# Performance work log

Measured on AMD Instinct MI355X. Metric: run time of the kernel, lower is better.

The kernel has to match this reference:

```python
import jax, jax.numpy as jnp
import numpy as np

N = 50000   # total nodes
E = 800000  # total edges (avg degree 16)
D = 128     # input_dim == hidden_dim
G = 256     # graphs in batch
C = 16      # output classes
L = 5       # num_layers
BN_EPS = 1e-5


def setup_inputs() -> dict:
    key = jax.random.key(0)
    ks = jax.random.split(key, 8)
    s = 1.0 / np.sqrt(D)
    return {
        "x": jax.random.normal(ks[0], (N, D), dtype=jnp.float32),
        "eps": jnp.zeros((L - 1,), dtype=jnp.float32),
        "W1": jax.random.normal(ks[1], (L - 1, D, D), dtype=jnp.float32) * s,
        "b1": jnp.zeros((L - 1, D), dtype=jnp.float32),
        "g1": jnp.ones((L - 1, D), dtype=jnp.float32),
        "beta1": jnp.zeros((L - 1, D), dtype=jnp.float32),
        "W2": jax.random.normal(ks[2], (L - 1, D, D), dtype=jnp.float32) * s,
        "b2": jnp.zeros((L - 1, D), dtype=jnp.float32),
        "g2": jnp.ones((L - 1, D), dtype=jnp.float32),
        "beta2": jnp.zeros((L - 1, D), dtype=jnp.float32),
        "Wp": jax.random.normal(ks[3], (L, D, C), dtype=jnp.float32) * s,
        "bp": jnp.zeros((L, C), dtype=jnp.float32),
        "edge_src": jax.random.randint(ks[4], (E,), 0, N),
        "edge_dst": jax.random.randint(ks[5], (E,), 0, N),
        "graph_ids": jnp.sort(jax.random.randint(ks[6], (N,), 0, G)),
    }


def _bn(x, g, b):
    # BatchNorm1d in training mode: biased batch statistics over the node axis
    m = jnp.mean(x, axis=0)
    v = jnp.mean(jnp.square(x - m), axis=0)
    return g * (x - m) * jax.lax.rsqrt(v + BN_EPS) + b


def reference(x, eps, W1, b1, g1, beta1, W2, b2, g2, beta2, Wp, bp,
              edge_src, edge_dst, graph_ids):
    hidden_representations = [x]
    h = x
    for l in range(L - 1):
        # spmm(adj, h): gather neighbor features along edges, scatter-add to dst
        pooled = jax.ops.segment_sum(h[edge_src], edge_dst, num_segments=N)
        pooled = pooled + (1.0 + eps[l]) * h  # learn_eps branch
        # MLP (num_mlp_layers=2): Linear+BN+ReLU, then Linear
        z = jax.nn.relu(_bn(pooled @ W1[l] + b1[l], g1[l], beta1[l]))
        z = z @ W2[l] + b2[l]
        # outer BN + ReLU
        h = jax.nn.relu(_bn(z, g2[l], beta2[l]))
        hidden_representations.append(h)

    out = jnp.zeros((G, C), dtype=x.dtype)
    for l, hl in enumerate(hidden_representations):
        # graph_pool spmm: sum-pool node features per graph
        pooled_h = jax.ops.segment_sum(hl, graph_ids, num_segments=G)
        out = out + pooled_h @ Wp[l] + bp[l]  # dropout p=0 -> identity
    return out
```

## Files before the change

kernel.cpp:

```cpp
#include <hip/hip_runtime.h>

#define N_NODES  50000
#define N_EDGES  800000
#define DIM      128
#define N_GRAPHS 256
#define N_CLASSES 16
#define N_LAYERS 5
#define BN_EPS   1e-5f

#define GEMM_BM 64
#define LDSP 136

typedef short bf16x8 __attribute__((ext_vector_type(8)));
typedef float f32x4  __attribute__((ext_vector_type(4)));

__device__ __forceinline__ float bf2f(unsigned short u) {
    unsigned int x = ((unsigned int)u) << 16;
    return __builtin_bit_cast(float, x);
}
__device__ __forceinline__ unsigned short f2bf(float f) {
    unsigned int x = __builtin_bit_cast(unsigned int, f);
    x += 0x7fffu + ((x >> 16) & 1u);
    return (unsigned short)(x >> 16);
}
__device__ __forceinline__ float lo16(unsigned int v) { return bf2f((unsigned short)(v & 0xffffu)); }
__device__ __forceinline__ float hi16(unsigned int v) { return bf2f((unsigned short)(v >> 16)); }
__device__ __forceinline__ unsigned int pack16(float a, float b) {
    return (unsigned int)f2bf(a) | ((unsigned int)f2bf(b) << 16);
}


__global__ void deg_kernel(const int* __restrict__ dst, int* __restrict__ deg, int e_count) {
    int e = blockIdx.x * blockDim.x + threadIdx.x;
    if (e < e_count) atomicAdd(&deg[dst[e]], 1);
}

__global__ void fill_csr_kernel(const int* __restrict__ src, const int* __restrict__ dst,
                                int* __restrict__ cursor, int* __restrict__ csr, int e_count) {
    int e = blockIdx.x * blockDim.x + threadIdx.x;
    if (e < e_count) {
        int d = dst[e];
        int p = atomicAdd(&cursor[d], 1);
        csr[p] = src[e];
    }
}

__global__ void gbound_kernel(const int* __restrict__ gid, int* __restrict__ gptr, int n, int G) {
    int i = blockIdx.x * blockDim.x + threadIdx.x;
    if (i >= n) return;
    int cur = gid[i];
    int prev = (i == 0) ? -1 : gid[i - 1];
    for (int g = prev + 1; g <= cur; ++g) gptr[g] = i;
    if (i == n - 1) {
        for (int g = cur + 1; g <= G; ++g) gptr[g] = n;
    }
}

__global__ void zrow_kernel(unsigned short* __restrict__ a, unsigned short* __restrict__ b) {
    int t = threadIdx.x;
    uint2 z = make_uint2(0u, 0u);
    if (t < 32) ((uint2*)(a + (size_t)N_NODES * DIM))[t] = z;
    else        ((uint2*)(b + (size_t)N_NODES * DIM))[t - 32] = z;
}


__global__ __launch_bounds__(1024) void scan_part_kernel(const int* __restrict__ in,
                                                         int* __restrict__ part, int n) {
    __shared__ int red[16];
    int tid = threadIdx.x;
    int i = blockIdx.x * 1024 + tid;
    int v = (i < n) ? in[i] : 0;
#pragma unroll
    for (int d = 1; d < 64; d <<= 1) v += __shfl_xor(v, d, 64);
    int lane = tid & 63, w = tid >> 6;
    if (lane == 0) red[w] = v;
    __syncthreads();
    if (tid == 0) {
        int s = 0;
#pragma unroll
        for (int k = 0; k < 16; ++k) s += red[k];
        part[blockIdx.x] = s;
    }
}

__global__ void scan_mid_kernel(int* __restrict__ part, int nb,
                                int* __restrict__ total_out, int total_idx) {
    int lane = threadIdx.x;
    int orig = (lane < nb) ? part[lane] : 0;
    int v = orig;
#pragma unroll
    for (int d = 1; d < 64; d <<= 1) {
        int t = __shfl_up(v, d, 64);
        if (lane >= d) v += t;
    }
    if (lane < nb) part[lane] = v - orig;
    if (lane == 63) total_out[total_idx] = v;
}

__global__ __launch_bounds__(1024) void scan_final_kernel(const int* __restrict__ in,
                                                          const int* __restrict__ part,
                                                          int* __restrict__ rowptr,
                                                          int* __restrict__ cursor, int n) {
    __shared__ int woff[16];
    int tid = threadIdx.x;
    int i = blockIdx.x * 1024 + tid;
    int v = (i < n) ? in[i] : 0;
    int lane = tid & 63, w = tid >> 6;
    int x = v;
#pragma unroll
    for (int d = 1; d < 64; d <<= 1) {
        int t = __shfl_up(x, d, 64);
        if (lane >= d) x += t;
    }
    if (lane == 63) woff[w] = x;
    __syncthreads();
    if (tid == 0) {
        int s = 0;
#pragma unroll
        for (int k = 0; k < 16; ++k) { int t = woff[k]; woff[k] = s; s += t; }
    }
    __syncthreads();
    int excl = part[blockIdx.x] + woff[w] + x - v;
    if (i < n) { rowptr[i] = excl; cursor[i] = excl; }
}


__global__ void f2b_kernel(const float* __restrict__ in, unsigned short* __restrict__ outp,
                           int n4d, int n4t) {
    int i = blockIdx.x * blockDim.x + threadIdx.x;
    if (i >= n4t) return;
    uint2 o = make_uint2(0u, 0u);
    if (i < n4d) {
        float4 v = ((const float4*)in)[i];
        o = make_uint2(pack16(v.x, v.y), pack16(v.z, v.w));
    }
    ((uint2*)outp)[i] = o;
}

__global__ void wconv_kernel(const float* __restrict__ W, unsigned short* __restrict__ Wt, int nmat) {
    int t = blockIdx.x * blockDim.x + threadIdx.x;
    if (t >= nmat * DIM * DIM) return;
    int m = t >> 14;
    int rem = t & 16383;
    int k = rem >> 7;
    int c = rem & 127;
    Wt[((size_t)m << 14) + (size_t)c * DIM + k] = f2bf(W[t]);
}


__device__ __forceinline__ void gemm_core8(
    unsigned short (*As)[LDSP], const unsigned short* __restrict__ Wt,
    unsigned short* __restrict__ Z, float* __restrict__ colsum, float* __restrict__ colsumsq,
    int nrows, int row0, int tid)
{
    int wid = tid >> 6, lane = tid & 63;
    int mq = wid & 3, ch = wid >> 2;
    int m0 = mq * 16;
    int lrow = lane & 15;
    int lk = (lane >> 4) * 8;

    f32x4 acc[4];
#pragma unroll
    for (int n = 0; n < 4; ++n) acc[n] = (f32x4){0.f, 0.f, 0.f, 0.f};

#pragma unroll
    for (int kk = 0; kk < 4; ++kk) {
        int k0 = kk * 32;
        bf16x8 a = *(const bf16x8*)&As[m0 + lrow][k0 + lk];
#pragma unroll
        for (int n = 0; n < 4; ++n) {
            bf16x8 b = *(const bf16x8*)(Wt + (size_t)(ch * 64 + n * 16 + lrow) * DIM + k0 + lk);
            acc[n] = __builtin_amdgcn_mfma_f32_16x16x32_bf16(a, b, acc[n], 0, 0, 0);
        }
    }

    int r0 = row0 + m0 + (lane >> 4) * 4;
    float sarr[4], qarr[4];
#pragma unroll
    for (int n = 0; n < 4; ++n) {
        int col = ch * 64 + n * 16 + lrow;
        float s = 0.f, q = 0.f;
#pragma unroll
        for (int j = 0; j < 4; ++j) {
            float v = acc[n][j];
            int row = r0 + j;
            if (row < nrows) Z[(size_t)row * DIM + col] = f2bf(v);
            s += v; q += v * v;
        }
        s += __shfl_xor(s, 16); q += __shfl_xor(q, 16);
        s += __shfl_xor(s, 32); q += __shfl_xor(q, 32);
        sarr[n] = s; qarr[n] = q;
    }

    __syncthreads();
    float* red = (float*)&As[0][0];
    if (lane < 16) {
#pragma unroll
        for (int n = 0; n < 4; ++n) {
            int col = ch * 64 + n * 16 + lrow;
            red[wid * 256 + col]       = sarr[n];
            red[wid * 256 + 128 + col] = qarr[n];
        }
    }
    __syncthreads();
    if (tid < 128) {
        int col = tid;
        int base = (col >> 6) * 4 * 256;
        float ts = red[base + col] + red[base + 256 + col]
                 + red[base + 512 + col] + red[base + 768 + col];
        float tq = red[base + 128 + col] + red[base + 384 + col]
                 + red[base + 640 + col] + red[base + 896 + col];
        atomicAdd(&colsum[col], ts);
        atomicAdd(&colsumsq[col], tq);
    }
}


__global__ __launch_bounds__(512) void gemmA_kernel(
    const unsigned short* __restrict__ h, const int* __restrict__ rowptr,
    const int* __restrict__ csr, const float* __restrict__ epsArr, int l,
    const unsigned short* __restrict__ Wt, unsigned short* __restrict__ Z,
    float* __restrict__ stats, int nrows)
{
    __shared__ __attribute__((aligned(16))) unsigned short As[GEMM_BM][LDSP];
    int tid = threadIdx.x;
    int row0 = blockIdx.x * GEMM_BM;
    int wid = tid >> 6, lane = tid & 63;
    int sub = lane >> 4, chunk = lane & 15;
    float ep = 1.0f + epsArr[l];

    for (int i = 0; i < 8; ++i) {
        int node = row0 + wid * 8 + i;
        float a8[8];
#pragma unroll
        for (int j = 0; j < 8; ++j) a8[j] = 0.f;
        if (node < nrows) {
            int beg = rowptr[node], end = rowptr[node + 1];
            int e0 = beg + sub;
            int sidx[8];
#pragma unroll
            for (int k = 0; k < 8; ++k) {
                int ee = e0 + k * 4;
                int ec = (ee < N_EDGES) ? ee : (N_EDGES - 1);
                int sv = csr[ec];
                sidx[k] = (ee < end) ? sv : N_NODES;
            }
            bf16x8 v[8];
#pragma unroll
            for (int k = 0; k < 8; ++k)
                v[k] = *(const bf16x8*)(h + (size_t)sidx[k] * DIM + chunk * 8);
#pragma unroll
            for (int k = 0; k < 8; ++k)
#pragma unroll
                for (int j = 0; j < 8; ++j)
                    a8[j] += bf2f((unsigned short)v[k][j]);
            for (int e = beg + 32 + sub; e < end; e += 4) {
                int sv = csr[e];
                bf16x8 vv = *(const bf16x8*)(h + (size_t)sv * DIM + chunk * 8);
#pragma unroll
                for (int j = 0; j < 8; ++j) a8[j] += bf2f((unsigned short)vv[j]);
            }
#pragma unroll
            for (int j = 0; j < 8; ++j) {
                a8[j] += __shfl_xor(a8[j], 16);
                a8[j] += __shfl_xor(a8[j], 32);
            }
            bf16x8 hv = *(const bf16x8*)(h + (size_t)node * DIM + chunk * 8);
#pragma unroll
            for (int j = 0; j < 8; ++j) a8[j] += ep * bf2f((unsigned short)hv[j]);
        }
        if (sub == 0) {
            bf16x8 o;
#pragma unroll
            for (int j = 0; j < 8; ++j) o[j] = (short)f2bf(a8[j]);
            *(bf16x8*)&As[wid * 8 + i][chunk * 8] = o;
        }
    }
    __syncthreads();
    gemm_core8(As, Wt, Z, stats, stats + 128, nrows, row0, tid);
}


__global__ __launch_bounds__(512) void gemmB_kernel(
    const unsigned short* __restrict__ Zin, const float* __restrict__ statsIn,
    const float* __restrict__ g, const float* __restrict__ beta,
    const unsigned short* __restrict__ Wt, unsigned short* __restrict__ Zout,
    float* __restrict__ statsOut, int nrows)
{
    __shared__ __attribute__((aligned(16))) unsigned short As[GEMM_BM][LDSP];
    __shared__ float abn[DIM], shbn[DIM];
    int tid = threadIdx.x;
    int row0 = blockIdx.x * GEMM_BM;

    if (tid < DIM) {
        const float invN = 1.0f / (float)N_NODES;
        float m = statsIn[tid] * invN;
        float var = statsIn[128 + tid] * invN - m * m;
        float s = g[tid] * rsqrtf(var + BN_EPS);
        abn[tid] = s;
        shbn[tid] = beta[tid] - s * m;
    }
    __syncthreads();

#pragma unroll
    for (int it = 0; it < 2; ++it) {
        int c = tid + it * 512;
        int r = c >> 4, kc = c & 15;
        bf16x8 o = {0, 0, 0, 0, 0, 0, 0, 0};
        if (row0 + r < nrows) {
            bf16x8 v = *(const bf16x8*)(Zin + (size_t)(row0 + r) * DIM + kc * 8);
#pragma unroll
            for (int cc = 0; cc < 8; ++cc) {
                int col = kc * 8 + cc;
                float f = bf2f((unsigned short)v[cc]);
                f = fmaxf(fmaf(abn[col], f, shbn[col]), 0.f);
                o[cc] = (short)f2bf(f);
            }
        }
        *(bf16x8*)&As[r][kc * 8] = o;
    }
    __syncthreads();
    gemm_core8(As, Wt, Zout, statsOut, statsOut + 128, nrows, row0, tid);
}


__global__ __launch_bounds__(256) void bnpool_kernel(
    const unsigned short* __restrict__ Zin, const float* __restrict__ stats,
    const float* __restrict__ g, const float* __restrict__ beta,
    const int* __restrict__ gid, unsigned short* __restrict__ hout,
    float* __restrict__ pooled, int nrows)
{
    __shared__ float abn[DIM], shbn[DIM];
    int tid = threadIdx.x;
    if (tid < DIM) {
        const float invN = 1.0f / (float)N_NODES;
        float m = stats[tid] * invN;
        float var = stats[128 + tid] * invN - m * m;
        float s = g[tid] * rsqrtf(var + BN_EPS);
        abn[tid] = s;
        shbn[tid] = beta[tid] - s * m;
    }
    __syncthreads();

    int row0 = blockIdx.x * GEMM_BM;
    int lane = tid & 63, w = tid >> 6;
    int c0 = lane * 2;
    float a0 = abn[c0], a1 = abn[c0 + 1], s0 = shbn[c0], s1 = shbn[c0 + 1];
    const unsigned int* Z2 = (const unsigned int*)Zin;
    unsigned int* H2 = (unsigned int*)hout;

    float px = 0.f, py = 0.f;
    int gcur = -1;
    for (int i = 0; i < 16; ++i) {
        int r = row0 + w * 16 + i;
        if (r >= nrows) break;
        int gg = gid[r];
        if (gg != gcur) {
            if (gcur >= 0) {
                atomicAdd(&pooled[(size_t)gcur * DIM + c0], px);
                atomicAdd(&pooled[(size_t)gcur * DIM + c0 + 1], py);
            }
            gcur = gg; px = 0.f; py = 0.f;
        }
        unsigned int v = Z2[(size_t)r * 64 + lane];
        float f0 = fmaxf(fmaf(a0, lo16(v), s0), 0.f);
        float f1 = fmaxf(fmaf(a1, hi16(v), s1), 0.f);
        unsigned int o = pack16(f0, f1);
        H2[(size_t)r * 64 + lane] = o;
        px += lo16(o);
        py += hi16(o);
    }
    if (gcur >= 0) {
        atomicAdd(&pooled[(size_t)gcur * DIM + c0], px);
        atomicAdd(&pooled[(size_t)gcur * DIM + c0 + 1], py);
    }
}


__global__ __launch_bounds__(256) void pool_kernel(
    const float* __restrict__ h, const int* __restrict__ gptr, float* __restrict__ outp)
{
    __shared__ float red[DIM];
    int g = blockIdx.x;
    int c = threadIdx.x & 127;
    int half = threadIdx.x >> 7;
    int beg = gptr[g], end = gptr[g + 1];
    float acc = 0.f;
    for (int n = beg + half; n < end; n += 2) acc += h[(size_t)n * DIM + c];
    if (half == 1) red[c] = acc;
    __syncthreads();
    if (half == 0) outp[(size_t)g * DIM + c] = acc + red[c];
}


__global__ __launch_bounds__(256) void final_kernel(
    const float* __restrict__ pooledH, const float* __restrict__ Wp,
    const float* __restrict__ bp, float* __restrict__ outp)
{
    int t = blockIdx.x * blockDim.x + threadIdx.x;
    if (t >= N_GRAPHS * N_CLASSES) return;
    int g = t >> 4, c = t & 15;
    float acc = 0.f;
    for (int l = 0; l < N_LAYERS; ++l) {
        const float* ph = pooledH + ((size_t)l * N_GRAPHS + g) * DIM;
        const float* w = Wp + (size_t)l * DIM * N_CLASSES + c;
        float a = 0.f;
        for (int k = 0; k < DIM; ++k) a = fmaf(ph[k], w[k * N_CLASSES], a);
        acc += a + bp[l * N_CLASSES + c];
    }
    outp[t] = acc;
}


extern "C" void kernel_launch(void* const* d_in, const int* in_sizes, int n_in,
                              void* d_out, int out_size, void* d_ws, size_t ws_size,
                              hipStream_t stream) {
    const float* x     = (const float*)d_in[0];
    const float* eps   = (const float*)d_in[1];
    const float* W1    = (const float*)d_in[2];
    const float* g1    = (const float*)d_in[4];
    const float* beta1 = (const float*)d_in[5];
    const float* W2    = (const float*)d_in[6];
    const float* g2    = (const float*)d_in[8];
    const float* beta2 = (const float*)d_in[9];
    const float* Wp    = (const float*)d_in[10];
    const float* bp    = (const float*)d_in[11];
    const int*   esrc  = (const int*)d_in[12];
    const int*   edst  = (const int*)d_in[13];
    const int*   gid   = (const int*)d_in[14];
    float* outp = (float*)d_out;

    char* ws = (char*)d_ws;
    size_t off = 0;
    auto alloc = [&](size_t bytes) {
        char* p = ws + off;
        off = (off + bytes + 255) & ~(size_t)255;
        return p;
    };
    unsigned short* xb  = (unsigned short*)alloc((size_t)(N_NODES + 1) * DIM * 2);
    unsigned short* B0  = (unsigned short*)alloc((size_t)(N_NODES + 1) * DIM * 2);
    unsigned short* B1  = (unsigned short*)alloc((size_t)(N_NODES + 1) * DIM * 2);
    unsigned short* ZB  = (unsigned short*)alloc((size_t)N_NODES * DIM * 2);
    unsigned short* Z2B = (unsigned short*)alloc((size_t)N_NODES * DIM * 2);
    unsigned short* Wt1 = (unsigned short*)alloc((size_t)(N_LAYERS - 1) * DIM * DIM * 2);
    unsigned short* Wt2 = (unsigned short*)alloc((size_t)(N_LAYERS - 1) * DIM * DIM * 2);
    int*   csr     = (int*)alloc((size_t)N_EDGES * 4);
    int*   deg     = (int*)alloc((N_NODES + 1) * 4);
    int*   rowptr  = (int*)alloc((N_NODES + 1) * 4);
    int*   cursor  = (int*)alloc((N_NODES + 1) * 4);
    int*   part    = (int*)alloc(64 * 4);
    int*   growptr = (int*)alloc(300 * 4);
    float* stats   = (float*)alloc(8 * 256 * 4);
    float* pooledH = (float*)alloc((size_t)N_LAYERS * N_GRAPHS * DIM * 4);

    hipMemsetAsync(deg, 0, N_NODES * 4, stream);
    hipMemsetAsync(stats, 0, 8 * 256 * 4, stream);
    hipMemsetAsync(pooledH, 0, (size_t)N_LAYERS * N_GRAPHS * DIM * 4, stream);

    const int nsb = (N_NODES + 1023) / 1024;
    deg_kernel<<<(N_EDGES + 255) / 256, 256, 0, stream>>>(edst, deg, N_EDGES);
    scan_part_kernel<<<nsb, 1024, 0, stream>>>(deg, part, N_NODES);
    scan_mid_kernel<<<1, 64, 0, stream>>>(part, nsb, rowptr, N_NODES);
    scan_final_kernel<<<nsb, 1024, 0, stream>>>(deg, part, rowptr, cursor, N_NODES);
    fill_csr_kernel<<<(N_EDGES + 255) / 256, 256, 0, stream>>>(esrc, edst, cursor, csr, N_EDGES);
    gbound_kernel<<<(N_NODES + 255) / 256, 256, 0, stream>>>(gid, growptr, N_NODES, N_GRAPHS);
    zrow_kernel<<<1, 64, 0, stream>>>(B0, B1);

    const int n4d = N_NODES * DIM / 4;
    const int n4t = (N_NODES + 1) * DIM / 4;
    f2b_kernel<<<(n4t + 255) / 256, 256, 0, stream>>>(x, xb, n4d, n4t);
    wconv_kernel<<<((N_LAYERS - 1) * DIM * DIM + 255) / 256, 256, 0, stream>>>(W1, Wt1, N_LAYERS - 1);
    wconv_kernel<<<((N_LAYERS - 1) * DIM * DIM + 255) / 256, 256, 0, stream>>>(W2, Wt2, N_LAYERS - 1);

    pool_kernel<<<N_GRAPHS, 256, 0, stream>>>(x, growptr, pooledH);

    const int ngrid = (N_NODES + GEMM_BM - 1) / GEMM_BM;
    unsigned short* hb = xb;
    unsigned short* nb = B0;
    for (int l = 0; l < N_LAYERS - 1; ++l) {
        gemmA_kernel<<<ngrid, 512, 0, stream>>>(
            hb, rowptr, csr, eps, l, Wt1 + (size_t)l * DIM * DIM, ZB,
            stats + (size_t)(2 * l) * 256, N_NODES);
        gemmB_kernel<<<ngrid, 512, 0, stream>>>(
            ZB, stats + (size_t)(2 * l) * 256, g1 + l * DIM, beta1 + l * DIM,
            Wt2 + (size_t)l * DIM * DIM, Z2B, stats + (size_t)(2 * l + 1) * 256, N_NODES);
        bnpool_kernel<<<ngrid, 256, 0, stream>>>(
            Z2B, stats + (size_t)(2 * l + 1) * 256, g2 + l * DIM, beta2 + l * DIM,
            gid, nb, pooledH + (size_t)(l + 1) * N_GRAPHS * DIM, N_NODES);

        hb = nb;
        nb = (hb == B0) ? B1 : B0;
    }

    final_kernel<<<(N_GRAPHS * N_CLASSES + 255) / 256, 256, 0, stream>>>(pooledH, Wp, bp, outp);
}
```

Measured before the change: 680.4 us.

## Merge setup kernels and gather two nodes per wavefront in aggregation

Folds the degree count and graph-boundary computation into one kernel, and merges the x/W bf16 conversions and layer-0 pooling into a single multi-role launch, cutting the number of kernel launches. In the aggregation GEMM, each wavefront now gathers two nodes at once, with two lanes per feature chunk instead of four, and unrolls over the first 16 edges. This is meant to give more memory-level parallelism across nodes for the average degree of 16 and to drop one shuffle stage. The tradeoff is a longer serial tail loop for high-degree nodes and less edge-level parallelism per node.

Result: slower. 700.9 us (+3.0%).

```diff
diff --git a/kernel.cpp b/kernel.cpp
--- a/kernel.cpp
+++ b/kernel.cpp
@@ -30,9 +30,17 @@
 }
 
 
-__global__ void deg_kernel(const int* __restrict__ dst, int* __restrict__ deg, int e_count) {
-    int e = blockIdx.x * blockDim.x + threadIdx.x;
-    if (e < e_count) atomicAdd(&deg[dst[e]], 1);
+__global__ void degbound_kernel(const int* __restrict__ dst, int* __restrict__ deg,
+                                const int* __restrict__ gid, int* __restrict__ gptr) {
+    int i = blockIdx.x * blockDim.x + threadIdx.x;
+    if (i < N_EDGES) atomicAdd(&deg[dst[i]], 1);
+    if (i < N_NODES) {
+        int cur = gid[i];
+        int prev = (i == 0) ? -1 : gid[i - 1];
+        for (int g = prev + 1; g <= cur; ++g) gptr[g] = i;
+        if (i == N_NODES - 1)
+            for (int g = cur + 1; g <= N_GRAPHS; ++g) gptr[g] = N_NODES;
+    }
 }
 
 __global__ void fill_csr_kernel(const int* __restrict__ src, const int* __restrict__ dst,
@@ -42,17 +50,6 @@
         int d = dst[e];
         int p = atomicAdd(&cursor[d], 1);
         csr[p] = src[e];
-    }
-}
-
-__global__ void gbound_kernel(const int* __restrict__ gid, int* __restrict__ gptr, int n, int G) {
-    int i = blockIdx.x * blockDim.x + threadIdx.x;
-    if (i >= n) return;
-    int cur = gid[i];
-    int prev = (i == 0) ? -1 : gid[i - 1];
-    for (int g = prev + 1; g <= cur; ++g) gptr[g] = i;
-    if (i == n - 1) {
-        for (int g = cur + 1; g <= G; ++g) gptr[g] = n;
     }
 }
 
@@ -125,26 +122,50 @@
 }
 
 
-__global__ void f2b_kernel(const float* __restrict__ in, unsigned short* __restrict__ outp,
-                           int n4d, int n4t) {
-    int i = blockIdx.x * blockDim.x + threadIdx.x;
-    if (i >= n4t) return;
-    uint2 o = make_uint2(0u, 0u);
-    if (i < n4d) {
-        float4 v = ((const float4*)in)[i];
-        o = make_uint2(pack16(v.x, v.y), pack16(v.z, v.w));
-    }
-    ((uint2*)outp)[i] = o;
-}
-
-__global__ void wconv_kernel(const float* __restrict__ W, unsigned short* __restrict__ Wt, int nmat) {
-    int t = blockIdx.x * blockDim.x + threadIdx.x;
-    if (t >= nmat * DIM * DIM) return;
-    int m = t >> 14;
-    int rem = t & 16383;
-    int k = rem >> 7;
-    int c = rem & 127;
-    Wt[((size_t)m << 14) + (size_t)c * DIM + k] = f2bf(W[t]);
+#define CVT_F2B_BLOCKS 2048
+#define CVT_W_BLOCKS   64
+
+__global__ __launch_bounds__(256) void convert_kernel(
+    const float* __restrict__ x, unsigned short* __restrict__ xb,
+    const float* __restrict__ W1, const float* __restrict__ W2,
+    unsigned short* __restrict__ Wt1, unsigned short* __restrict__ Wt2,
+    const int* __restrict__ gptr, float* __restrict__ pool0)
+{
+    __shared__ float red[DIM];
+    int b = blockIdx.x, tid = threadIdx.x;
+    if (b < N_GRAPHS) {
+        int c = tid & 127;
+        int half = tid >> 7;
+        int beg = gptr[b], end = gptr[b + 1];
+        float acc = 0.f;
+        for (int n = beg + half; n < end; n += 2) acc += x[(size_t)n * DIM + c];
+        if (half == 1) red[c] = acc;
+        __syncthreads();
+        if (half == 0) pool0[(size_t)b * DIM + c] = acc + red[c];
+    } else if (b < N_GRAPHS + CVT_F2B_BLOCKS) {
+        const int total_data = N_NODES * DIM / 4;
+        const int total = (N_NODES + 1) * DIM / 4;
+        const int stride = CVT_F2B_BLOCKS * 256;
+        for (int i = (b - N_GRAPHS) * 256 + tid; i < total; i += stride) {
+            uint2 o = make_uint2(0u, 0u);
+            if (i < total_data) {
+                float4 v = ((const float4*)x)[i];
+                o = make_uint2(pack16(v.x, v.y), pack16(v.z, v.w));
+            }
+            ((uint2*)xb)[i] = o;
+        }
+    } else {
+        const int total = (N_LAYERS - 1) * DIM * DIM;
+        const int stride = CVT_W_BLOCKS * 256;
+        for (int t = (b - N_GRAPHS - CVT_F2B_BLOCKS) * 256 + tid; t < total; t += stride) {
+            int m = t >> 14;
+            int k = (t & 16383) >> 7;
+            int c = t & 127;
+            size_t dstp = ((size_t)m << 14) + (size_t)c * DIM + k;
+            Wt1[dstp] = f2bf(W1[t]);
+            Wt2[dstp] = f2bf(W2[t]);
+        }
+    }
 }
 
 
@@ -226,54 +247,60 @@
     int tid = threadIdx.x;
     int row0 = blockIdx.x * GEMM_BM;
     int wid = tid >> 6, lane = tid & 63;
-    int sub = lane >> 4, chunk = lane & 15;
+    int nsel = lane >> 5, esub = (lane >> 4) & 1, chunk = lane & 15;
     float ep = 1.0f + epsArr[l];
 
-    for (int i = 0; i < 8; ++i) {
-        int node = row0 + wid * 8 + i;
+    for (int t = 0; t < 4; ++t) {
+        int node = row0 + wid * 8 + t * 2 + nsel;
+        bool valid = node < nrows;
+        int beg = 0, end = 0;
+        if (valid) { beg = rowptr[node]; end = rowptr[node + 1]; }
+
+        int sidx[8];
+#pragma unroll
+        for (int k = 0; k < 8; ++k) {
+            int ee = beg + esub + 2 * k;
+            int ec = (ee < N_EDGES) ? ee : (N_EDGES - 1);
+            int sv = csr[ec];
+            sidx[k] = (valid && ee < end) ? sv : N_NODES;
+        }
+        bf16x8 v[8];
+#pragma unroll
+        for (int k = 0; k < 8; ++k)
+            v[k] = *(const bf16x8*)(h + (size_t)sidx[k] * DIM + chunk * 8);
+
         float a8[8];
 #pragma unroll
         for (int j = 0; j < 8; ++j) a8[j] = 0.f;
-        if (node < nrows) {
-            int beg = rowptr[node], end = rowptr[node + 1];
-            int e0 = beg + sub;
-            int sidx[8];
-#pragma unroll
-            for (int k = 0; k < 8; ++k) {
-                int ee = e0 + k * 4;
-                int ec = (ee < N_EDGES) ? ee : (N_EDGES - 1);
-                int sv = csr[ec];
-                sidx[k] = (ee < end) ? sv : N_NODES;
-            }
-            bf16x8 v[8];
-#pragma unroll
-            for (int k = 0; k < 8; ++k)
-                v[k] = *(const bf16x8*)(h + (size_t)sidx[k] * DIM + chunk * 8);
-#pragma unroll
-            for (int k = 0; k < 8; ++k)
-#pragma unroll
-                for (int j = 0; j < 8; ++j)
-                    a8[j] += bf2f((unsigned short)v[k][j]);
-            for (int e = beg + 32 + sub; e < end; e += 4) {
+#pragma unroll
+        for (int k = 0; k < 8; ++k)
+#pragma unroll
+            for (int j = 0; j < 8; ++j)
+                a8[j] += bf2f((unsigned short)v[k][j]);
+
+        if (valid) {
+            for (int e = beg + 16 + esub; e < end; e += 2) {
                 int sv = csr[e];
                 bf16x8 vv = *(const bf16x8*)(h + (size_t)sv * DIM + chunk * 8);
 #pragma unroll
                 for (int j = 0; j < 8; ++j) a8[j] += bf2f((unsigned short)vv[j]);
             }
-#pragma unroll
-            for (int j = 0; j < 8; ++j) {
-                a8[j] += __shfl_xor(a8[j], 16);
-                a8[j] += __shfl_xor(a8[j], 32);
-            }
+        }
+
+#pragma unroll
+        for (int j = 0; j < 8; ++j) a8[j] += __shfl_xor(a8[j], 16);
+
+        if (valid) {
             bf16x8 hv = *(const bf16x8*)(h + (size_t)node * DIM + chunk * 8);
 #pragma unroll
             for (int j = 0; j < 8; ++j) a8[j] += ep * bf2f((unsigned short)hv[j]);
         }
-        if (sub == 0) {
+
+        if (esub == 0) {
             bf16x8 o;
 #pragma unroll
             for (int j = 0; j < 8; ++j) o[j] = (short)f2bf(a8[j]);
-            *(bf16x8*)&As[wid * 8 + i][chunk * 8] = o;
+            *(bf16x8*)&As[wid * 8 + t * 2 + nsel][chunk * 8] = o;
         }
     }
     __syncthreads();
@@ -374,22 +401,6 @@
         atomicAdd(&pooled[(size_t)gcur * DIM + c0], px);
         atomicAdd(&pooled[(size_t)gcur * DIM + c0 + 1], py);
     }
-}
-
-
-__global__ __launch_bounds__(256) void pool_kernel(
-    const float* __restrict__ h, const int* __restrict__ gptr, float* __restrict__ outp)
-{
-    __shared__ float red[DIM];
-    int g = blockIdx.x;
-    int c = threadIdx.x & 127;
-    int half = threadIdx.x >> 7;
-    int beg = gptr[g], end = gptr[g + 1];
-    float acc = 0.f;
-    for (int n = beg + half; n < end; n += 2) acc += h[(size_t)n * DIM + c];
-    if (half == 1) red[c] = acc;
-    __syncthreads();
-    if (half == 0) outp[(size_t)g * DIM + c] = acc + red[c];
 }
 
 
@@ -458,38 +469,33 @@
     hipMemsetAsync(pooledH, 0, (size_t)N_LAYERS * N_GRAPHS * DIM * 4, stream);
 
     const int nsb = (N_NODES + 1023) / 1024;
-    deg_kernel<<<(N_EDGES + 255) / 256, 256, 0, stream>>>(edst, deg, N_EDGES);
+    degbound_kernel<<<(N_EDGES + 255) / 256, 256, 0, stream>>>(edst, deg, gid, growptr);
     scan_part_kernel<<<nsb, 1024, 0, stream>>>(deg, part, N_NODES);
     scan_mid_kernel<<<1, 64, 0, stream>>>(part, nsb, rowptr, N_NODES);
     scan_final_kernel<<<nsb, 1024, 0, stream>>>(deg, part, rowptr, cursor, N_NODES);
     fill_csr_kernel<<<(N_EDGES + 255) / 256, 256, 0, stream>>>(esrc, edst, cursor, csr, N_EDGES);
-    gbound_kernel<<<(N_NODES + 255) / 256, 256, 0, stream>>>(gid, growptr, N_NODES, N_GRAPHS);
     zrow_kernel<<<1, 64, 0, stream>>>(B0, B1);
 
-    const int n4d = N_NODES * DIM / 4;
-    const int n4t = (N_NODES + 1) * DIM / 4;
-    f2b_kernel<<<(n4t + 255) / 256, 256, 0, stream>>>(x, xb, n4d, n4t);
-    wconv_kernel<<<((N_LAYERS - 1) * DIM * DIM + 255) / 256, 256, 0, stream>>>(W1, Wt1, N_LAYERS - 1);
-    wconv_kernel<<<((N_LAYERS - 1) * DIM * DIM + 255) / 256, 256, 0, stream>>>(W2, Wt2, N_LAYERS - 1);
-
-    pool_kernel<<<N_GRAPHS, 256, 0, stream>>>(x, growptr, pooledH);
+    convert_kernel<<<N_GRAPHS + CVT_F2B_BLOCKS + CVT_W_BLOCKS, 256, 0, stream>>>(
+        x, xb, W1, W2, Wt1, Wt2, growptr, pooledH);
 
     const int ngrid = (N_NODES + GEMM_BM - 1) / GEMM_BM;
-    unsigned short* hb = xb;
+    const unsigned short* hb = xb;
     unsigned short* nb = B0;
     for (int l = 0; l < N_LAYERS - 1; ++l) {
+        float* statsA = stats + (size_t)(2 * l) * 256;
+        float* statsB = stats + (size_t)(2 * l + 1) * 256;
         gemmA_kernel<<<ngrid, 512, 0, stream>>>(
-            hb, rowptr, csr, eps, l, Wt1 + (size_t)l * DIM * DIM, ZB,
-            stats + (size_t)(2 * l) * 256, N_NODES);
+            hb, rowptr, csr, eps, l, Wt1 + (size_t)l * DIM * DIM, ZB, statsA, N_NODES);
         gemmB_kernel<<<ngrid, 512, 0, stream>>>(
-            ZB, stats + (size_t)(2 * l) * 256, g1 + l * DIM, beta1 + l * DIM,
-            Wt2 + (size_t)l * DIM * DIM, Z2B, stats + (size_t)(2 * l + 1) * 256, N_NODES);
+            ZB, statsA, g1 + (size_t)l * DIM, beta1 + (size_t)l * DIM,
+            Wt2 + (size_t)l * DIM * DIM, Z2B, statsB, N_NODES);
         bnpool_kernel<<<ngrid, 256, 0, stream>>>(
-            Z2B, stats + (size_t)(2 * l + 1) * 256, g2 + l * DIM, beta2 + l * DIM,
+            Z2B, statsB, g2 + (size_t)l * DIM, beta2 + (size_t)l * DIM,
             gid, nb, pooledH + (size_t)(l + 1) * N_GRAPHS * DIM, N_NODES);
 
         hb = nb;
-        nb = (hb == B0) ? B1 : B0;
+        nb = (nb == B0) ? B1 : B0;
     }
 
     final_kernel<<<(N_GRAPHS * N_CLASSES + 255) / 256, 256, 0, stream>>>(pooledH, Wp, bp, outp);
```
